# Kernel tuning notes

Measured on AMD Instinct MI355X. Metric: run time of the kernel, lower is better.

## Reference

```python
import jax, jax.numpy as jnp
import numpy as np

NUM_RELATIONS = 2
NUM_NODES = 100000


def rgcn_conv(x, edge_index, edge_type, weight, root, bias):
    """PyG RGCNConv with default aggr='mean':
    out[i] = bias + x[i] @ root + sum_r mean_{j in N_r(i)} (x[j] @ W_r)
    x: [N, Cin], edge_index: [2, E], weight: [R, Cin, Cout], root: [Cin, Cout]."""
    src, dst = edge_index[0], edge_index[1]
    x_src = x[src]                      # [E, Cin] gather
    out = x @ root + bias               # [N, Cout]
    for r in range(NUM_RELATIONS):      # small fixed loop over relations
        mask = (edge_type == r).astype(x.dtype)          # [E]
        msg = (x_src @ weight[r]) * mask[:, None]        # [E, Cout]
        agg = jax.ops.segment_sum(msg, dst, num_segments=NUM_NODES)
        deg = jax.ops.segment_sum(mask, dst, num_segments=NUM_NODES)
        out = out + agg / jnp.maximum(deg, 1.0)[:, None]
    return out


def setup_inputs() -> dict:
    key = jax.random.key(0)
    ks = jax.random.split(key, 16)
    Cin, Chid, Cout = 128, 256, 128
    E = 400000
    inp = {
        "x0": jax.random.normal(ks[0], (50000, 128), jnp.float32),
        "x1": jax.random.normal(ks[1], (50000, 64), jnp.float32),
        "edge_index": jax.random.randint(ks[2], (2, E), 0, NUM_NODES),
        "edge_type": jax.random.randint(ks[3], (E,), 0, NUM_RELATIONS),
        "dec_index": jax.random.randint(ks[4], (2, 100000), 0, NUM_NODES),
        # per-node-type input projections (Linear as x @ W + b)
        "lin0_w": jax.random.normal(ks[5], (128, Cin), jnp.float32) * 0.05,
        "lin0_b": jnp.zeros((Cin,), jnp.float32),
        "lin1_w": jax.random.normal(ks[6], (64, Cin), jnp.float32) * 0.05,
        "lin1_b": jnp.zeros((Cin,), jnp.float32),
        # RGCN layer 1
        "conv1_w": jax.random.normal(ks[7], (NUM_RELATIONS, Cin, Chid), jnp.float32) * 0.05,
        "conv1_root": jax.random.normal(ks[8], (Cin, Chid), jnp.float32) * 0.05,
        "conv1_b": jnp.zeros((Chid,), jnp.float32),
        # RGCN layer 2
        "conv2_w": jax.random.normal(ks[9], (NUM_RELATIONS, Chid, Cout), jnp.float32) * 0.05,
        "conv2_root": jax.random.normal(ks[10], (Chid, Cout), jnp.float32) * 0.05,
        "conv2_b": jnp.zeros((Cout,), jnp.float32),
        # decode head: Linear(2*Cout -> 1) + sigmoid
        "fc_w": jax.random.normal(ks[11], (2 * Cout, 1), jnp.float32) * 0.05,
        "fc_b": jnp.zeros((1,), jnp.float32),
    }
    return inp


def reference(x0, x1, edge_index, edge_type, dec_index,
              lin0_w, lin0_b, lin1_w, lin1_b,
              conv1_w, conv1_root, conv1_b,
              conv2_w, conv2_root, conv2_b,
              fc_w, fc_b):
    # trans_dimensions: per-type projection then concat along nodes
    x = jnp.concatenate([x0 @ lin0_w + lin0_b, x1 @ lin1_w + lin1_b], axis=0)  # [N, Cin]
    # encode (eval mode: dropout is identity)
    x = rgcn_conv(x, edge_index, edge_type, conv1_w, conv1_root, conv1_b)
    x = jax.nn.relu(x)
    z = rgcn_conv(x, edge_index, edge_type, conv2_w, conv2_root, conv2_b)
    # decode
    pair = jnp.concatenate([z[dec_index[0]], z[dec_index[1]]], axis=-1)  # [P, 2*Cout]
    return jax.nn.sigmoid(pair @ fc_w + fc_b)
```

## Files before the change

### kernel.cpp

```cpp
#include <hip/hip_runtime.h>
#include <hip/hip_bf16.h>
#include <math.h>

#define N_NODES 100000
#define N_EDGES 400000
#define N_PAIRS 100000
#define NBINS   200000

typedef short short8_t __attribute__((ext_vector_type(8)));
typedef float f32x4    __attribute__((ext_vector_type(4)));

__device__ __forceinline__ ushort f2bf(float f) {
    uint u = __float_as_uint(f);
    u += 0x7fffu + ((u >> 16) & 1u);
    return (ushort)(u >> 16);
}
__device__ __forceinline__ float bf2f(ushort b) {
    return __uint_as_float(((uint)b) << 16);
}
__device__ __forceinline__ uint packbf(float a, float b) {
    return (uint)f2bf(a) | ((uint)f2bf(b) << 16);
}

#define GLDS16(gp, lp) \
    __builtin_amdgcn_global_load_lds((const __attribute__((address_space(1))) uint*)(gp), \
                                     (__attribute__((address_space(3))) uint*)(lp), 16, 0, 0)

template<int N> __device__ __forceinline__ void waitvm() {
    if constexpr (N == 0)      asm volatile("s_waitcnt vmcnt(0)" ::: "memory");
    else if constexpr (N == 4) asm volatile("s_waitcnt vmcnt(4)" ::: "memory");
    else if constexpr (N == 8) asm volatile("s_waitcnt vmcnt(8)" ::: "memory");
}

__global__ void cast_kernel(const float* __restrict__ in, ushort* __restrict__ outp, int n4) {
    int i = blockIdx.x * 256 + threadIdx.x;
    int stride = gridDim.x * 256;
    for (; i < n4; i += stride) {
        float4 v = ((const float4*)in)[i];
        ushort4 o;
        o.x = f2bf(v.x); o.y = f2bf(v.y); o.z = f2bf(v.z); o.w = f2bf(v.w);
        ((ushort4*)outp)[i] = o;
    }
}

__global__ void wlin_kernel(const float* __restrict__ w, ushort* __restrict__ wt, int K) {
    int i = blockIdx.x * 256 + threadIdx.x;
    if (i >= 128 * K) return;
    int n = i / K, k = i - n * K;
    wt[i] = f2bf(w[(size_t)k * 128 + n]);
}
__global__ void wc1_kernel(const float* __restrict__ root, const float* __restrict__ w,
                           ushort* __restrict__ wt) {
    int i = blockIdx.x * 256 + threadIdx.x;
    if (i >= 256 * 384) return;
    int n = i / 384, k = i % 384;
    float v;
    if (k < 128) v = root[(size_t)k * 256 + n];
    else         v = w[(size_t)(k - 128) * 256 + n];
    wt[(size_t)n * 384 + k] = f2bf(v);
}
__global__ void wc2_kernel(const float* __restrict__ root, const float* __restrict__ w,
                           ushort* __restrict__ wt) {
    int i = blockIdx.x * 256 + threadIdx.x;
    if (i >= 384 * 256) return;
    int n = i / 256, k = i % 256;
    float v;
    if (n < 128) v = root[(size_t)k * 128 + n];
    else         v = w[((size_t)((n >> 7) - 1) * 256 + k) * 128 + (n & 127)];
    wt[(size_t)n * 256 + k] = f2bf(v);
}

__global__ void hist_kernel(const int* __restrict__ dst, const int* __restrict__ et,
                            int* __restrict__ cnt) {
    int e = blockIdx.x * 256 + threadIdx.x;
    if (e < N_EDGES) atomicAdd(&cnt[et[e] * N_NODES + dst[e]], 1);
}

__global__ __launch_bounds__(1024) void scan1_kernel(const int* __restrict__ cnt,
                                                     int* __restrict__ ptr,
                                                     int* __restrict__ aux) {
    __shared__ int s[1024];
    int i = blockIdx.x * 1024 + threadIdx.x;
    int v = (i < NBINS) ? cnt[i] : 0;
    s[threadIdx.x] = v;
    __syncthreads();
    for (int off = 1; off < 1024; off <<= 1) {
        int t = (threadIdx.x >= off) ? s[threadIdx.x - off] : 0;
        __syncthreads();
        s[threadIdx.x] += t;
        __syncthreads();
    }
    if (i < NBINS) ptr[i] = s[threadIdx.x] - v;
    if (threadIdx.x == 1023) aux[blockIdx.x] = s[1023];
}

__global__ void scan2_kernel(int* __restrict__ aux, int nblk) {
    __shared__ int s[256];
    int v = (threadIdx.x < nblk) ? aux[threadIdx.x] : 0;
    s[threadIdx.x] = v;
    __syncthreads();
    for (int off = 1; off < 256; off <<= 1) {
        int t = (threadIdx.x >= off) ? s[threadIdx.x - off] : 0;
        __syncthreads();
        s[threadIdx.x] += t;
        __syncthreads();
    }
    if (threadIdx.x < nblk) aux[threadIdx.x] = s[threadIdx.x] - v;
}

__global__ void scan3_kernel(const int* __restrict__ aux, int* __restrict__ ptr,
                             int* __restrict__ cursor) {
    int i = blockIdx.x * 256 + threadIdx.x;
    if (i < NBINS) {
        int val = ptr[i] + aux[i >> 10];
        ptr[i] = val;
        cursor[i] = val;
    }
    if (i == 0) ptr[NBINS] = N_EDGES;
}

__global__ void fill_kernel(const int* __restrict__ src, const int* __restrict__ dst,
                            const int* __restrict__ et, int* __restrict__ cursor,
                            int* __restrict__ esorted) {
    int e = blockIdx.x * 256 + threadIdx.x;
    if (e < N_EDGES) {
        int b = et[e] * N_NODES + dst[e];
        int pos = atomicAdd(&cursor[b], 1);
        esorted[pos] = src[e];
    }
}

__global__ void gather1_kernel(const int* __restrict__ ptr, const int* __restrict__ es,
                               ushort* __restrict__ A1) {
    int d = blockIdx.x * 4 + (threadIdx.x >> 6);
    if (d >= N_NODES) return;
    int lane = threadIdx.x & 63;
    int p0 = ptr[d],           p1 = ptr[d + 1];
    int q0 = ptr[N_NODES + d], q1 = ptr[N_NODES + d + 1];
    int n0 = p1 - p0, n1 = q1 - q0;
    int n  = n0 > n1 ? n0 : n1;
    float a0 = 0, a1 = 0, b0 = 0, b1 = 0;
    for (int k = 0; k < n; k += 2) {
        uint v00 = 0, v01 = 0, v10 = 0, v11 = 0;
        if (k < n0)     v00 = *(const uint*)(A1 + (size_t)es[p0 + k] * 384 + lane * 2);
        if (k + 1 < n0) v01 = *(const uint*)(A1 + (size_t)es[p0 + k + 1] * 384 + lane * 2);
        if (k < n1)     v10 = *(const uint*)(A1 + (size_t)es[q0 + k] * 384 + lane * 2);
        if (k + 1 < n1) v11 = *(const uint*)(A1 + (size_t)es[q0 + k + 1] * 384 + lane * 2);
        a0 += bf2f((ushort)(v00 & 0xffffu)) + bf2f((ushort)(v01 & 0xffffu));
        a1 += bf2f((ushort)(v00 >> 16))     + bf2f((ushort)(v01 >> 16));
        b0 += bf2f((ushort)(v10 & 0xffffu)) + bf2f((ushort)(v11 & 0xffffu));
        b1 += bf2f((ushort)(v10 >> 16))     + bf2f((ushort)(v11 >> 16));
    }
    float i0 = n0 ? 1.0f / (float)n0 : 0.0f;
    float i1 = n1 ? 1.0f / (float)n1 : 0.0f;
    uint* row = (uint*)(A1 + (size_t)d * 384);
    row[64  + lane] = packbf(a0 * i0, a1 * i0);
    row[128 + lane] = packbf(b0 * i1, b1 * i1);
}

__global__ void combine2_kernel(const int* __restrict__ ptr, const int* __restrict__ es,
                                const ushort* __restrict__ H, ushort* __restrict__ zb) {
    int d = blockIdx.x * 4 + (threadIdx.x >> 6);
    if (d >= N_NODES) return;
    int lane = threadIdx.x & 63;
    int p0 = ptr[d],           p1 = ptr[d + 1];
    int q0 = ptr[N_NODES + d], q1 = ptr[N_NODES + d + 1];
    int n0 = p1 - p0, n1 = q1 - q0;
    int n  = n0 > n1 ? n0 : n1;
    uint rv = *(const uint*)(H + (size_t)d * 384 + lane * 2);
    float r0 = bf2f((ushort)(rv & 0xffffu)), r1 = bf2f((ushort)(rv >> 16));
    float a0 = 0, a1 = 0, b0 = 0, b1 = 0;
    for (int k = 0; k < n; k += 2) {
        uint v00 = 0, v01 = 0, v10 = 0, v11 = 0;
        if (k < n0)     v00 = *(const uint*)(H + (size_t)es[p0 + k] * 384 + 128 + lane * 2);
        if (k + 1 < n0) v01 = *(const uint*)(H + (size_t)es[p0 + k + 1] * 384 + 128 + lane * 2);
        if (k < n1)     v10 = *(const uint*)(H + (size_t)es[q0 + k] * 384 + 256 + lane * 2);
        if (k + 1 < n1) v11 = *(const uint*)(H + (size_t)es[q0 + k + 1] * 384 + 256 + lane * 2);
        a0 += bf2f((ushort)(v00 & 0xffffu)) + bf2f((ushort)(v01 & 0xffffu));
        a1 += bf2f((ushort)(v00 >> 16))     + bf2f((ushort)(v01 >> 16));
        b0 += bf2f((ushort)(v10 & 0xffffu)) + bf2f((ushort)(v11 & 0xffffu));
        b1 += bf2f((ushort)(v10 >> 16))     + bf2f((ushort)(v11 >> 16));
    }
    float i0 = n0 ? 1.0f / (float)n0 : 0.0f;
    float i1 = n1 ? 1.0f / (float)n1 : 0.0f;
    uint* orow = (uint*)(zb + (size_t)d * 128);
    orow[lane] = packbf(r0 + a0 * i0 + b0 * i1, r1 + a1 * i0 + b1 * i1);
}

template<int KTOT, int NP, int OST, int BIASN, bool RELU>
__global__ __launch_bounds__(256)
void mfma_gemm_kernel(const ushort* __restrict__ A, const ushort* __restrict__ Wt,
                      const float* __restrict__ bias, ushort* __restrict__ outp,
                      int nrows, int mtiles) {
    __shared__ short As[3][128 * 32];
    __shared__ short Bs[3][128 * 32];
    const int t = threadIdx.x;
    const int lane = t & 63, w = t >> 6;
    const int wr = w >> 1, wc = w & 1;
    const int l15 = lane & 15, l4 = lane >> 4;

    const int nwg = mtiles * NP;
    const int q = nwg >> 3, r = nwg & 7;
    const int orig = blockIdx.x;
    const int xcd = orig & 7;
    const int work = (xcd < r ? xcd * (q + 1) : r * (q + 1) + (xcd - r) * q) + (orig >> 3);
    const int mt = work / NP;
    const int m0 = mt * 128;
    const int n0 = (work - mt * NP) * 128;

    const int arow = t >> 2;
    const int swc = ((t & 3) ^ ((arow >> 1) & 3)) * 8;
    int rg0 = m0 + arow;      if (rg0 >= nrows) rg0 = nrows - 1;
    int rg1 = m0 + arow + 64; if (rg1 >= nrows) rg1 = nrows - 1;
    const ushort* ap0 = A + (size_t)rg0 * KTOT + swc;
    const ushort* ap1 = A + (size_t)rg1 * KTOT + swc;
    const ushort* bp0 = Wt + (size_t)(n0 + arow) * KTOT + swc;
    const ushort* bp1 = Wt + (size_t)(n0 + arow + 64) * KTOT + swc;

#define STAGE(slot, kg) do { \
        GLDS16(ap0 + (kg), &As[slot][t * 8]); \
        GLDS16(ap1 + (kg), &As[slot][(t + 256) * 8]); \
        GLDS16(bp0 + (kg), &Bs[slot][t * 8]); \
        GLDS16(bp1 + (kg), &Bs[slot][(t + 256) * 8]); \
    } while (0)

    f32x4 acc[4][4];
#pragma unroll
    for (int j = 0; j < 4; j++) {
        int col = n0 + wc * 64 + j * 16 + l15;
        float bv = (col < BIASN) ? bias[col] : 0.0f;
        f32x4 tmp = {bv, bv, bv, bv};
#pragma unroll
        for (int i = 0; i < 4; i++) acc[i][j] = tmp;
    }

    const int xr = (l4 ^ ((l15 >> 1) & 3)) * 8;

    constexpr int NSTEP = KTOT / 32;
    STAGE(0, 0);
    if (NSTEP > 1) STAGE(1, 32);
    for (int ks = 0; ks < NSTEP; ks++) {
        const int slot = ks % 3;
        if (ks + 2 < NSTEP) {
            STAGE((ks + 2) % 3, (ks + 2) * 32);
            waitvm<8>();
        } else if (ks + 1 < NSTEP) {
            waitvm<4>();
        } else {
            waitvm<0>();
        }
        asm volatile("s_barrier" ::: "memory");
        short8_t af[4], bfr[4];
#pragma unroll
        for (int i = 0; i < 4; i++)
            af[i] = *(short8_t*)&As[slot][(wr * 64 + i * 16 + l15) * 32 + xr];
#pragma unroll
        for (int j = 0; j < 4; j++)
            bfr[j] = *(short8_t*)&Bs[slot][(wc * 64 + j * 16 + l15) * 32 + xr];
#pragma unroll
        for (int i = 0; i < 4; i++)
#pragma unroll
            for (int j = 0; j < 4; j++)
                acc[i][j] = __builtin_amdgcn_mfma_f32_16x16x32_bf16(af[i], bfr[j], acc[i][j], 0, 0, 0);
        asm volatile("s_barrier" ::: "memory");
    }
#undef STAGE

#pragma unroll
    for (int i = 0; i < 4; i++) {
#pragma unroll
        for (int r2 = 0; r2 < 4; r2++) {
            int row = m0 + wr * 64 + i * 16 + l4 * 4 + r2;
            if (row < nrows) {
#pragma unroll
                for (int j = 0; j < 4; j++) {
                    int col = n0 + wc * 64 + j * 16 + l15;
                    float v = acc[i][j][r2];
                    if (RELU) v = fmaxf(v, 0.0f);
                    outp[(size_t)row * OST + col] = f2bf(v);
                }
            }
        }
    }
}

__global__ void decode_kernel(const ushort* __restrict__ zb, const int* __restrict__ dec,
                              const float* __restrict__ fcw, const float* __restrict__ fcb,
                              float* __restrict__ out) {
    int wid  = blockIdx.x * 4 + (threadIdx.x >> 6);
    int lane = threadIdx.x & 63;
    if (wid >= N_PAIRS) return;
    int s = dec[wid];
    int d = dec[N_PAIRS + wid];
    uint vs = ((const uint*)(zb + (size_t)s * 128))[lane];
    uint vd = ((const uint*)(zb + (size_t)d * 128))[lane];
    float v = bf2f((ushort)(vs & 0xffffu)) * fcw[2 * lane]
            + bf2f((ushort)(vs >> 16))     * fcw[2 * lane + 1]
            + bf2f((ushort)(vd & 0xffffu)) * fcw[128 + 2 * lane]
            + bf2f((ushort)(vd >> 16))     * fcw[128 + 2 * lane + 1];
#pragma unroll
    for (int off = 32; off > 0; off >>= 1) v += __shfl_down(v, off);
    if (lane == 0) out[wid] = 1.0f / (1.0f + expf(-(v + fcb[0])));
}

extern "C" void kernel_launch(void* const* d_in, const int* in_sizes, int n_in,
                              void* d_out, int out_size, void* d_ws, size_t ws_size,
                              hipStream_t stream) {
    const float* x0        = (const float*)d_in[0];
    const float* x1        = (const float*)d_in[1];
    const int*   edge_idx  = (const int*)  d_in[2];
    const int*   edge_type = (const int*)  d_in[3];
    const int*   dec_index = (const int*)  d_in[4];
    const float* lin0_w    = (const float*)d_in[5];
    const float* lin0_b    = (const float*)d_in[6];
    const float* lin1_w    = (const float*)d_in[7];
    const float* lin1_b    = (const float*)d_in[8];
    const float* conv1_w   = (const float*)d_in[9];
    const float* conv1_root= (const float*)d_in[10];
    const float* conv1_b   = (const float*)d_in[11];
    const float* conv2_w   = (const float*)d_in[12];
    const float* conv2_root= (const float*)d_in[13];
    const float* conv2_b   = (const float*)d_in[14];
    const float* fc_w      = (const float*)d_in[15];
    const float* fc_b      = (const float*)d_in[16];
    float* out = (float*)d_out;

    char* W = (char*)d_ws;
    ushort* A1    = (ushort*)(W + 0);
    ushort* H     = (ushort*)(W + 0);
    ushort* y1    = (ushort*)(W + 76800000);
    ushort* zb    = (ushort*)(W + 76800000);
    int*    cnt   = (int*)   (W + 128000000);
    int*    ptrb  = (int*)   (W + 128800000);
    int*    cursor= (int*)   (W + 129600016);
    int*    aux   = (int*)   (W + 130400016);
    int*    esort = (int*)   (W + 130404112);
    ushort* wc1   = (ushort*)(W + 132004112);
    ushort* wc2   = (ushort*)(W + 132200720);
    ushort* wl0   = (ushort*)(W + 132397328);
    ushort* wl1   = (ushort*)(W + 132430096);
    ushort* x0bf  = (ushort*)(W + 132446480);
    ushort* x1bf  = (ushort*)(W + 145246480);

    const int* esrc = edge_idx;
    const int* edst = edge_idx + N_EDGES;

    hipMemsetAsync(cnt, 0, (size_t)NBINS * sizeof(int), stream);

    cast_kernel<<<2048, 256, 0, stream>>>(x0, x0bf, 50000 * 128 / 4);
    cast_kernel<<<2048, 256, 0, stream>>>(x1, x1bf, 50000 * 64 / 4);
    wlin_kernel<<<64, 256, 0, stream>>>(lin0_w, wl0, 128);
    wlin_kernel<<<32, 256, 0, stream>>>(lin1_w, wl1, 64);
    wc1_kernel<<<(256 * 384 + 255) / 256, 256, 0, stream>>>(conv1_root, conv1_w, wc1);
    wc2_kernel<<<(384 * 256 + 255) / 256, 256, 0, stream>>>(conv2_root, conv2_w, wc2);

    hist_kernel<<<(N_EDGES + 255) / 256, 256, 0, stream>>>(edst, edge_type, cnt);
    scan1_kernel<<<(NBINS + 1023) / 1024, 1024, 0, stream>>>(cnt, ptrb, aux);
    scan2_kernel<<<1, 256, 0, stream>>>(aux, (NBINS + 1023) / 1024);
    scan3_kernel<<<(NBINS + 255) / 256, 256, 0, stream>>>(aux, ptrb, cursor);
    fill_kernel<<<(N_EDGES + 255) / 256, 256, 0, stream>>>(esrc, edst, edge_type,
                                                           cursor, esort);

    mfma_gemm_kernel<128, 1, 384, 128, false>
        <<<391, 256, 0, stream>>>(x0bf, wl0, lin0_b, A1, 50000, 391);
    mfma_gemm_kernel<64, 1, 384, 128, false>
        <<<391, 256, 0, stream>>>(x1bf, wl1, lin1_b,
                                  A1 + (size_t)50000 * 384, 50000, 391);

    gather1_kernel<<<(N_NODES + 3) / 4, 256, 0, stream>>>(ptrb, esort, A1);
    mfma_gemm_kernel<384, 2, 256, 256, true>
        <<<1564, 256, 0, stream>>>(A1, wc1, conv1_b, y1, N_NODES, 782);

    mfma_gemm_kernel<256, 3, 384, 128, false>
        <<<2346, 256, 0, stream>>>(y1, wc2, conv2_b, H, N_NODES, 782);
    combine2_kernel<<<(N_NODES + 3) / 4, 256, 0, stream>>>(ptrb, esort, H, zb);

    decode_kernel<<<(N_PAIRS + 3) / 4, 256, 0, stream>>>(zb, dec_index, fc_w, fc_b, out);
}
```

Measured before the change: 274.3 us.

## Fuse prep kernels and projection GEMMs, unroll gather loops by four

Merges the two casts, the four weight-transpose kernels and the histogram memset into one grid-stride prep kernel. The two input-projection GEMMs become a single launch that dispatches on block index. The gather and combine loops now issue four neighbor loads per relation per iteration instead of two. This removes several launches and tail gaps and adds memory-level parallelism in the gathers, at the cost of more registers and a branchy prep kernel.

```diff
diff --git a/kernel.cpp b/kernel.cpp
--- a/kernel.cpp
+++ b/kernel.cpp
@@ -32,42 +32,47 @@
     else if constexpr (N == 8) asm volatile("s_waitcnt vmcnt(8)" ::: "memory");
 }
 
-__global__ void cast_kernel(const float* __restrict__ in, ushort* __restrict__ outp, int n4) {
+#define PREP_TOTAL 2671184
+__global__ void prep_kernel(const float* __restrict__ x0, const float* __restrict__ x1,
+                            const float* __restrict__ l0w, const float* __restrict__ l1w,
+                            const float* __restrict__ c1r, const float* __restrict__ c1w,
+                            const float* __restrict__ c2r, const float* __restrict__ c2w,
+                            ushort* __restrict__ x0bf, ushort* __restrict__ x1bf,
+                            ushort* __restrict__ wl0, ushort* __restrict__ wl1,
+                            ushort* __restrict__ wc1, ushort* __restrict__ wc2,
+                            int* __restrict__ cnt) {
     int i = blockIdx.x * 256 + threadIdx.x;
-    int stride = gridDim.x * 256;
-    for (; i < n4; i += stride) {
-        float4 v = ((const float4*)in)[i];
-        ushort4 o;
-        o.x = f2bf(v.x); o.y = f2bf(v.y); o.z = f2bf(v.z); o.w = f2bf(v.w);
-        ((ushort4*)outp)[i] = o;
-    }
-}
-
-__global__ void wlin_kernel(const float* __restrict__ w, ushort* __restrict__ wt, int K) {
-    int i = blockIdx.x * 256 + threadIdx.x;
-    if (i >= 128 * K) return;
-    int n = i / K, k = i - n * K;
-    wt[i] = f2bf(w[(size_t)k * 128 + n]);
-}
-__global__ void wc1_kernel(const float* __restrict__ root, const float* __restrict__ w,
-                           ushort* __restrict__ wt) {
-    int i = blockIdx.x * 256 + threadIdx.x;
-    if (i >= 256 * 384) return;
-    int n = i / 384, k = i % 384;
-    float v;
-    if (k < 128) v = root[(size_t)k * 256 + n];
-    else         v = w[(size_t)(k - 128) * 256 + n];
-    wt[(size_t)n * 384 + k] = f2bf(v);
-}
-__global__ void wc2_kernel(const float* __restrict__ root, const float* __restrict__ w,
-                           ushort* __restrict__ wt) {
-    int i = blockIdx.x * 256 + threadIdx.x;
-    if (i >= 384 * 256) return;
-    int n = i / 256, k = i % 256;
-    float v;
-    if (n < 128) v = root[(size_t)k * 128 + n];
-    else         v = w[((size_t)((n >> 7) - 1) * 256 + k) * 128 + (n & 127)];
-    wt[(size_t)n * 256 + k] = f2bf(v);
+    const int stride = gridDim.x * 256;
+    for (; i < PREP_TOTAL; i += stride) {
+        int j = i;
+        if (j < 1600000) {
+            float4 v = ((const float4*)x0)[j];
+            ushort4 o; o.x = f2bf(v.x); o.y = f2bf(v.y); o.z = f2bf(v.z); o.w = f2bf(v.w);
+            ((ushort4*)x0bf)[j] = o;
+        } else if ((j -= 1600000) < 800000) {
+            float4 v = ((const float4*)x1)[j];
+            ushort4 o; o.x = f2bf(v.x); o.y = f2bf(v.y); o.z = f2bf(v.z); o.w = f2bf(v.w);
+            ((ushort4*)x1bf)[j] = o;
+        } else if ((j -= 800000) < 16384) {
+            int n = j >> 7, k = j & 127;
+            wl0[j] = f2bf(l0w[(size_t)k * 128 + n]);
+        } else if ((j -= 16384) < 8192) {
+            int n = j >> 6, k = j & 63;
+            wl1[j] = f2bf(l1w[(size_t)k * 128 + n]);
+        } else if ((j -= 8192) < 98304) {
+            int n = j / 384, k = j % 384;
+            float v = (k < 128) ? c1r[(size_t)k * 256 + n] : c1w[(size_t)(k - 128) * 256 + n];
+            wc1[(size_t)n * 384 + k] = f2bf(v);
+        } else if ((j -= 98304) < 98304) {
+            int n = j >> 8, k = j & 255;
+            float v = (n < 128) ? c2r[(size_t)k * 128 + n]
+                                : c2w[((size_t)((n >> 7) - 1) * 256 + k) * 128 + (n & 127)];
+            wc2[(size_t)n * 256 + k] = f2bf(v);
+        } else {
+            j -= 98304;
+            ((int4*)cnt)[j] = make_int4(0, 0, 0, 0);
+        }
+    }
 }
 
 __global__ void hist_kernel(const int* __restrict__ dst, const int* __restrict__ et,
@@ -140,16 +145,25 @@
     int n0 = p1 - p0, n1 = q1 - q0;
     int n  = n0 > n1 ? n0 : n1;
     float a0 = 0, a1 = 0, b0 = 0, b1 = 0;
-    for (int k = 0; k < n; k += 2) {
-        uint v00 = 0, v01 = 0, v10 = 0, v11 = 0;
-        if (k < n0)     v00 = *(const uint*)(A1 + (size_t)es[p0 + k] * 384 + lane * 2);
+    for (int k = 0; k < n; k += 4) {
+        uint v00 = 0, v01 = 0, v02 = 0, v03 = 0;
+        uint v10 = 0, v11 = 0, v12 = 0, v13 = 0;
+        if (k     < n0) v00 = *(const uint*)(A1 + (size_t)es[p0 + k]     * 384 + lane * 2);
         if (k + 1 < n0) v01 = *(const uint*)(A1 + (size_t)es[p0 + k + 1] * 384 + lane * 2);
-        if (k < n1)     v10 = *(const uint*)(A1 + (size_t)es[q0 + k] * 384 + lane * 2);
+        if (k + 2 < n0) v02 = *(const uint*)(A1 + (size_t)es[p0 + k + 2] * 384 + lane * 2);
+        if (k + 3 < n0) v03 = *(const uint*)(A1 + (size_t)es[p0 + k + 3] * 384 + lane * 2);
+        if (k     < n1) v10 = *(const uint*)(A1 + (size_t)es[q0 + k]     * 384 + lane * 2);
         if (k + 1 < n1) v11 = *(const uint*)(A1 + (size_t)es[q0 + k + 1] * 384 + lane * 2);
-        a0 += bf2f((ushort)(v00 & 0xffffu)) + bf2f((ushort)(v01 & 0xffffu));
-        a1 += bf2f((ushort)(v00 >> 16))     + bf2f((ushort)(v01 >> 16));
-        b0 += bf2f((ushort)(v10 & 0xffffu)) + bf2f((ushort)(v11 & 0xffffu));
-        b1 += bf2f((ushort)(v10 >> 16))     + bf2f((ushort)(v11 >> 16));
+        if (k + 2 < n1) v12 = *(const uint*)(A1 + (size_t)es[q0 + k + 2] * 384 + lane * 2);
+        if (k + 3 < n1) v13 = *(const uint*)(A1 + (size_t)es[q0 + k + 3] * 384 + lane * 2);
+        a0 += bf2f((ushort)(v00 & 0xffffu)) + bf2f((ushort)(v01 & 0xffffu))
+            + bf2f((ushort)(v02 & 0xffffu)) + bf2f((ushort)(v03 & 0xffffu));
+        a1 += bf2f((ushort)(v00 >> 16)) + bf2f((ushort)(v01 >> 16))
+            + bf2f((ushort)(v02 >> 16)) + bf2f((ushort)(v03 >> 16));
+        b0 += bf2f((ushort)(v10 & 0xffffu)) + bf2f((ushort)(v11 & 0xffffu))
+            + bf2f((ushort)(v12 & 0xffffu)) + bf2f((ushort)(v13 & 0xffffu));
+        b1 += bf2f((ushort)(v10 >> 16)) + bf2f((ushort)(v11 >> 16))
+            + bf2f((ushort)(v12 >> 16)) + bf2f((ushort)(v13 >> 16));
     }
     float i0 = n0 ? 1.0f / (float)n0 : 0.0f;
     float i1 = n1 ? 1.0f / (float)n1 : 0.0f;
@@ -170,16 +184,25 @@
     uint rv = *(const uint*)(H + (size_t)d * 384 + lane * 2);
     float r0 = bf2f((ushort)(rv & 0xffffu)), r1 = bf2f((ushort)(rv >> 16));
     float a0 = 0, a1 = 0, b0 = 0, b1 = 0;
-    for (int k = 0; k < n; k += 2) {
-        uint v00 = 0, v01 = 0, v10 = 0, v11 = 0;
-        if (k < n0)     v00 = *(const uint*)(H + (size_t)es[p0 + k] * 384 + 128 + lane * 2);
+    for (int k = 0; k < n; k += 4) {
+        uint v00 = 0, v01 = 0, v02 = 0, v03 = 0;
+        uint v10 = 0, v11 = 0, v12 = 0, v13 = 0;
+        if (k     < n0) v00 = *(const uint*)(H + (size_t)es[p0 + k]     * 384 + 128 + lane * 2);
         if (k + 1 < n0) v01 = *(const uint*)(H + (size_t)es[p0 + k + 1] * 384 + 128 + lane * 2);
-        if (k < n1)     v10 = *(const uint*)(H + (size_t)es[q0 + k] * 384 + 256 + lane * 2);
+        if (k + 2 < n0) v02 = *(const uint*)(H + (size_t)es[p0 + k + 2] * 384 + 128 + lane * 2);
+        if (k + 3 < n0) v03 = *(const uint*)(H + (size_t)es[p0 + k + 3] * 384 + 128 + lane * 2);
+        if (k     < n1) v10 = *(const uint*)(H + (size_t)es[q0 + k]     * 384 + 256 + lane * 2);
         if (k + 1 < n1) v11 = *(const uint*)(H + (size_t)es[q0 + k + 1] * 384 + 256 + lane * 2);
-        a0 += bf2f((ushort)(v00 & 0xffffu)) + bf2f((ushort)(v01 & 0xffffu));
-        a1 += bf2f((ushort)(v00 >> 16))     + bf2f((ushort)(v01 >> 16));
-        b0 += bf2f((ushort)(v10 & 0xffffu)) + bf2f((ushort)(v11 & 0xffffu));
-        b1 += bf2f((ushort)(v10 >> 16))     + bf2f((ushort)(v11 >> 16));
+        if (k + 2 < n1) v12 = *(const uint*)(H + (size_t)es[q0 + k + 2] * 384 + 256 + lane * 2);
+        if (k + 3 < n1) v13 = *(const uint*)(H + (size_t)es[q0 + k + 3] * 384 + 256 + lane * 2);
+        a0 += bf2f((ushort)(v00 & 0xffffu)) + bf2f((ushort)(v01 & 0xffffu))
+            + bf2f((ushort)(v02 & 0xffffu)) + bf2f((ushort)(v03 & 0xffffu));
+        a1 += bf2f((ushort)(v00 >> 16)) + bf2f((ushort)(v01 >> 16))
+            + bf2f((ushort)(v02 >> 16)) + bf2f((ushort)(v03 >> 16));
+        b0 += bf2f((ushort)(v10 & 0xffffu)) + bf2f((ushort)(v11 & 0xffffu))
+            + bf2f((ushort)(v12 & 0xffffu)) + bf2f((ushort)(v13 & 0xffffu));
+        b1 += bf2f((ushort)(v10 >> 16)) + bf2f((ushort)(v11 >> 16))
+            + bf2f((ushort)(v12 >> 16)) + bf2f((ushort)(v13 >> 16));
     }
     float i0 = n0 ? 1.0f / (float)n0 : 0.0f;
     float i1 = n1 ? 1.0f / (float)n1 : 0.0f;
@@ -187,26 +210,17 @@
     orow[lane] = packbf(r0 + a0 * i0 + b0 * i1, r1 + a1 * i0 + b1 * i1);
 }
 
-template<int KTOT, int NP, int OST, int BIASN, bool RELU>
-__global__ __launch_bounds__(256)
-void mfma_gemm_kernel(const ushort* __restrict__ A, const ushort* __restrict__ Wt,
-                      const float* __restrict__ bias, ushort* __restrict__ outp,
-                      int nrows, int mtiles) {
+template<int KTOT, int OST, int BIASN, bool RELU>
+__device__ __forceinline__
+void gemm_body(const ushort* __restrict__ A, const ushort* __restrict__ Wt,
+               const float* __restrict__ bias, ushort* __restrict__ outp,
+               int nrows, int m0, int n0) {
     __shared__ short As[3][128 * 32];
     __shared__ short Bs[3][128 * 32];
     const int t = threadIdx.x;
     const int lane = t & 63, w = t >> 6;
     const int wr = w >> 1, wc = w & 1;
     const int l15 = lane & 15, l4 = lane >> 4;
-
-    const int nwg = mtiles * NP;
-    const int q = nwg >> 3, r = nwg & 7;
-    const int orig = blockIdx.x;
-    const int xcd = orig & 7;
-    const int work = (xcd < r ? xcd * (q + 1) : r * (q + 1) + (xcd - r) * q) + (orig >> 3);
-    const int mt = work / NP;
-    const int m0 = mt * 128;
-    const int n0 = (work - mt * NP) * 128;
 
     const int arow = t >> 2;
     const int swc = ((t & 3) ^ ((arow >> 1) & 3)) * 8;
@@ -282,6 +296,34 @@
             }
         }
     }
+}
+
+template<int KTOT, int NP, int OST, int BIASN, bool RELU>
+__global__ __launch_bounds__(256)
+void mfma_gemm_kernel(const ushort* __restrict__ A, const ushort* __restrict__ Wt,
+                      const float* __restrict__ bias, ushort* __restrict__ outp,
+                      int nrows, int mtiles) {
+    const int nwg = mtiles * NP;
+    const int q = nwg >> 3, r = nwg & 7;
+    const int orig = blockIdx.x;
+    const int xcd = orig & 7;
+    const int work = (xcd < r ? xcd * (q + 1) : r * (q + 1) + (xcd - r) * q) + (orig >> 3);
+    const int mt = work / NP;
+    gemm_body<KTOT, OST, BIASN, RELU>(A, Wt, bias, outp, nrows,
+                                      mt * 128, (work - mt * NP) * 128);
+}
+
+__global__ __launch_bounds__(256)
+void proj_kernel(const ushort* __restrict__ x0bf, const ushort* __restrict__ x1bf,
+                 const ushort* __restrict__ wl0, const ushort* __restrict__ wl1,
+                 const float* __restrict__ l0b, const float* __restrict__ l1b,
+                 ushort* __restrict__ A1) {
+    if (blockIdx.x < 391)
+        gemm_body<128, 384, 128, false>(x0bf, wl0, l0b, A1, 50000,
+                                        blockIdx.x * 128, 0);
+    else
+        gemm_body<64, 384, 128, false>(x1bf, wl1, l1b, A1 + (size_t)50000 * 384, 50000,
+                                       (blockIdx.x - 391) * 128, 0);
 }
 
 __global__ void decode_kernel(const ushort* __restrict__ zb, const int* __restrict__ dec,
@@ -345,14 +387,9 @@
     const int* esrc = edge_idx;
     const int* edst = edge_idx + N_EDGES;
 
-    hipMemsetAsync(cnt, 0, (size_t)NBINS * sizeof(int), stream);
-
-    cast_kernel<<<2048, 256, 0, stream>>>(x0, x0bf, 50000 * 128 / 4);
-    cast_kernel<<<2048, 256, 0, stream>>>(x1, x1bf, 50000 * 64 / 4);
-    wlin_kernel<<<64, 256, 0, stream>>>(lin0_w, wl0, 128);
-    wlin_kernel<<<32, 256, 0, stream>>>(lin1_w, wl1, 64);
-    wc1_kernel<<<(256 * 384 + 255) / 256, 256, 0, stream>>>(conv1_root, conv1_w, wc1);
-    wc2_kernel<<<(384 * 256 + 255) / 256, 256, 0, stream>>>(conv2_root, conv2_w, wc2);
+    prep_kernel<<<2048, 256, 0, stream>>>(x0, x1, lin0_w, lin1_w,
+                                          conv1_root, conv1_w, conv2_root, conv2_w,
+                                          x0bf, x1bf, wl0, wl1, wc1, wc2, cnt);
 
     hist_kernel<<<(N_EDGES + 255) / 256, 256, 0, stream>>>(edst, edge_type, cnt);
     scan1_kernel<<<(NBINS + 1023) / 1024, 1024, 0, stream>>>(cnt, ptrb, aux);
@@ -361,11 +398,7 @@
     fill_kernel<<<(N_EDGES + 255) / 256, 256, 0, stream>>>(esrc, edst, edge_type,
                                                            cursor, esort);
 
-    mfma_gemm_kernel<128, 1, 384, 128, false>
-        <<<391, 256, 0, stream>>>(x0bf, wl0, lin0_b, A1, 50000, 391);
-    mfma_gemm_kernel<64, 1, 384, 128, false>
-        <<<391, 256, 0, stream>>>(x1bf, wl1, lin1_b,
-                                  A1 + (size_t)50000 * 384, 50000, 391);
+    proj_kernel<<<782, 256, 0, stream>>>(x0bf, x1bf, wl0, wl1, lin0_b, lin1_b, A1);
 
     gather1_kernel<<<(N_NODES + 3) / 4, 256, 0, stream>>>(ptrb, esort, A1);
     mfma_gemm_kernel<384, 2, 256, 256, true>
```

Measured after the change: 257.4 us. 6.2% less time.
